# Optimization experiments

Hardware: AMD Instinct MI355X
Metric: run time of the kernel (lower is better)

## Reference

```python
import jax, jax.numpy as jnp
import numpy as np

B, N, D = 256, 8192, 768
TEMP = 0.05          # CE temperature (temp init arg; CE losses are computed but NOT returned)
SUPCON_T = 0.07      # standard SupConLoss temperature (default in the repo's SupConLoss)


def _l2norm(x, eps=1e-12):
    # matches F.normalize(dim=-1): clamp of the norm by eps
    n = jnp.linalg.norm(x, axis=-1, keepdims=True)
    return x / jnp.maximum(n, eps)


def _supcon(feats, mem, labels, mem_labels):
    # SupConLoss(features, memory, targets, prototype_labels):
    # anchor-vs-memory logits, positives where labels match prototype labels.
    logits = feats @ mem.T / SUPCON_T                              # [B, N]
    logits = logits - jax.lax.stop_gradient(logits.max(axis=1, keepdims=True))
    log_prob = logits - jax.nn.logsumexp(logits, axis=1, keepdims=True)
    mask = (labels[:, None] == mem_labels[None, :]).astype(logits.dtype)
    mean_log_prob_pos = (mask * log_prob).sum(1) / jnp.maximum(mask.sum(1), 1.0)
    return -mean_log_prob_pos.mean()


def setup_inputs() -> dict:
    key = jax.random.key(0)
    k1, k2, k3, k4, k5, k6, k7, k8 = jax.random.split(key, 8)
    inputs_rgb = jax.random.normal(k1, (B, D), dtype=jnp.float32)
    inputs_ir = jax.random.normal(k2, (B, D), dtype=jnp.float32)
    targets_rgb = jax.random.randint(k3, (B,), 0, N)
    targets_ir = jax.random.randint(k4, (B,), 0, N)
    # memory banks are unit-normalized prototypes in practice
    features_rgb = _l2norm(jax.random.normal(k5, (N, D), dtype=jnp.float32))
    features_ir = _l2norm(jax.random.normal(k6, (N, D), dtype=jnp.float32))
    # prototype labels: permutations of arange(N) so cross-modal lookups always match
    prototype_labels_rgb = jax.random.permutation(k7, jnp.arange(N))
    prototype_labels_ir = jax.random.permutation(k8, jnp.arange(N))
    return {
        "inputs_rgb": inputs_rgb, "inputs_ir": inputs_ir,
        "targets_rgb": targets_rgb, "targets_ir": targets_ir,
        "features_rgb": features_rgb, "features_ir": features_ir,
        "prototype_labels_rgb": prototype_labels_rgb,
        "prototype_labels_ir": prototype_labels_ir,
    }


def reference(inputs_rgb, inputs_ir, targets_rgb, targets_ir,
              features_rgb, features_ir, prototype_labels_rgb, prototype_labels_ir):
    x_rgb = _l2norm(inputs_rgb)
    x_ir = _l2norm(inputs_ir)
    # cm_double forward matmuls -> CE losses are computed in torch but never returned
    # (dead w.r.t. the module's outputs), so they don't affect the returned values.
    loss_contr = (_supcon(x_rgb, features_rgb, targets_rgb, prototype_labels_rgb)
                  + _supcon(x_ir, features_ir, targets_ir, prototype_labels_ir))
    loss_contr_cross = (_supcon(x_rgb, features_ir, targets_rgb, prototype_labels_ir)
                        + _supcon(x_ir, features_rgb, targets_ir, prototype_labels_rgb))
    return (loss_contr, loss_contr_cross)
```

## Files before the change

### kernel.cpp

```cpp
#include <hip/hip_runtime.h>
#include <hip/hip_bf16.h>
#include <math.h>

#define Bsz 256
#define Nsz 8192
#define Dsz 768
#define NROWS 512
#define INV_T 14.2857142857f
#define NT 64
#define NCB (Nsz / NT)
#define KC 64
#define NSTG (Dsz / KC)

typedef __attribute__((ext_vector_type(4))) float f32x4;
typedef __attribute__((ext_vector_type(8))) short bf16x8;
typedef __attribute__((ext_vector_type(4))) short bf16x4;

__device__ __forceinline__ unsigned short f2bf(float f) {
    union { float f; unsigned u; } x; x.f = f;
    unsigned u = x.u;
    return (unsigned short)((u + 0x7fffu + ((u >> 16) & 1u)) >> 16);
}
__device__ __forceinline__ float bf2f(unsigned short u) {
    union { unsigned u; float f; } x; x.u = ((unsigned)u) << 16;
    return x.f;
}

__device__ __forceinline__ int fr_idx(int row, int k) {
    int rb = row >> 4, kc = k >> 5;
    int lane = (((k >> 3) & 3) << 4) | (row & 15);
    return (((rb * 24 + kc) << 6) | lane) * 8 + (k & 7);
}

__device__ __forceinline__ bf16x8 cvt8(float4 a, float4 b) {
    union { bf16x8 v; __hip_bfloat162 h[4]; } r;
    r.h[0] = __float22bfloat162_rn({a.x, a.y});
    r.h[1] = __float22bfloat162_rn({a.z, a.w});
    r.h[2] = __float22bfloat162_rn({b.x, b.y});
    r.h[3] = __float22bfloat162_rn({b.z, b.w});
    return r.v;
}

__global__ void k_prep(const float* __restrict__ xrgb, const float* __restrict__ xir,
                       const int* __restrict__ prgb, const int* __restrict__ pir,
                       unsigned short* __restrict__ xrm, unsigned short* __restrict__ xfr,
                       int* __restrict__ inv) {
    int b = blockIdx.x, t = threadIdx.x;
    if (b < NROWS) {
        const float* src = (b < Bsz) ? (xrgb + b * Dsz) : (xir + (b - Bsz) * Dsz);
        float v0 = src[t], v1 = src[t + 256], v2 = src[t + 512];
        float ss = v0 * v0 + v1 * v1 + v2 * v2;
        #pragma unroll
        for (int m = 1; m < 64; m <<= 1) ss += __shfl_xor(ss, m);
        __shared__ float w4[4];
        if ((t & 63) == 0) w4[t >> 6] = ss;
        __syncthreads();
        float tot = w4[0] + w4[1] + w4[2] + w4[3];
        float invn = 1.0f / fmaxf(sqrtf(tot), 1e-12f);
        unsigned short b0 = f2bf(v0 * invn), b1 = f2bf(v1 * invn), b2 = f2bf(v2 * invn);
        xrm[b * Dsz + t] = b0;
        xrm[b * Dsz + t + 256] = b1;
        xrm[b * Dsz + t + 512] = b2;
        xfr[fr_idx(b, t)] = b0;
        xfr[fr_idx(b, t + 256)] = b1;
        xfr[fr_idx(b, t + 512)] = b2;
    } else {
        int i = (b - NROWS) * 256 + t;
        if (i < Nsz) inv[prgb[i]] = i;
        else         inv[Nsz + pir[i - Nsz]] = i - Nsz;
    }
}

__global__ __launch_bounds__(512) void k_big(
    const float* __restrict__ Frgb, const float* __restrict__ Fir,
    const unsigned short* __restrict__ xfr,
    float* __restrict__ part_m, float* __restrict__ part_s) {
    __shared__ short Bs[2][NT * KC];
    int bid = blockIdx.x;
    int bank = bid >> 7;
    int cb = bid & (NCB - 1);
    const float* F = bank ? Fir : Frgb;
    int t = threadIdx.x;
    int w = t >> 6, lane = t & 63, lr = lane & 15, lg = lane >> 4;

    int scol = t >> 3, sj = t & 7;
    const float* sbase = F + (long)(cb * NT + scol) * Dsz + sj * 8;
    int swidx = scol * 64 + ((sj * 8) ^ ((scol & 7) << 3));

    f32x4 acc[4][4] = {};

    {
        float4 u = *(const float4*)sbase;
        float4 v = *(const float4*)(sbase + 4);
        *(bf16x8*)&Bs[0][swidx] = cvt8(u, v);
    }
    __syncthreads();

    for (int s = 0; s < NSTG; ++s) {
        int nxt = s + 1;
        float4 un, vn;
        if (nxt < NSTG) {
            const float* p = sbase + nxt * KC;
            un = *(const float4*)p;
            vn = *(const float4*)(p + 4);
        }
        const short* B0 = Bs[s & 1];
        #pragma unroll
        for (int h = 0; h < 2; ++h) {
            int kc = s * 2 + h;
            bf16x8 bfr[4];
            #pragma unroll
            for (int cf = 0; cf < 4; ++cf) {
                int col = cf * 16 + lr;
                int kloc = h * 32 + lg * 8;
                bfr[cf] = *(const bf16x8*)&B0[col * 64 + (kloc ^ ((col & 7) << 3))];
            }
            #pragma unroll
            for (int rf = 0; rf < 4; ++rf) {
                int rb = w * 4 + rf;
                bf16x8 af = *(const bf16x8*)&xfr[(((rb * 24 + kc) << 6) | lane) * 8];
                #pragma unroll
                for (int cf = 0; cf < 4; ++cf)
                    acc[rf][cf] = __builtin_amdgcn_mfma_f32_16x16x32_bf16(af, bfr[cf], acc[rf][cf], 0, 0, 0);
            }
        }
        if (nxt < NSTG)
            *(bf16x8*)&Bs[nxt & 1][swidx] = cvt8(un, vn);
        __syncthreads();
    }

    #pragma unroll
    for (int rf = 0; rf < 4; ++rf) {
        #pragma unroll
        for (int reg = 0; reg < 4; ++reg) {
            float v0 = acc[rf][0][reg] * INV_T, v1 = acc[rf][1][reg] * INV_T;
            float v2 = acc[rf][2][reg] * INV_T, v3 = acc[rf][3][reg] * INV_T;
            float mx = fmaxf(fmaxf(v0, v1), fmaxf(v2, v3));
            mx = fmaxf(mx, __shfl_xor(mx, 1));
            mx = fmaxf(mx, __shfl_xor(mx, 2));
            mx = fmaxf(mx, __shfl_xor(mx, 4));
            mx = fmaxf(mx, __shfl_xor(mx, 8));
            float sum = __expf(v0 - mx) + __expf(v1 - mx) + __expf(v2 - mx) + __expf(v3 - mx);
            sum += __shfl_xor(sum, 1); sum += __shfl_xor(sum, 2);
            sum += __shfl_xor(sum, 4); sum += __shfl_xor(sum, 8);
            if (lr == 0) {
                int row = w * 64 + rf * 16 + lg * 4 + reg;
                long o = (long)(bank * NROWS + row) * NCB + cb;
                part_m[o] = mx;
                part_s[o] = sum;
            }
        }
    }
}

__global__ void k_combine(const float* __restrict__ part_m, const float* __restrict__ part_s,
                          const float* __restrict__ Frgb, const float* __restrict__ Fir,
                          const int* __restrict__ trgb, const int* __restrict__ tir,
                          const unsigned short* __restrict__ xrm, const int* __restrict__ inv,
                          float* __restrict__ loss) {
    int gw = (blockIdx.x * blockDim.x + threadIdx.x) >> 6;
    int lane = threadIdx.x & 63;
    int bank = gw >> 9, r = gw & 511;
    const float* pm = part_m + (long)(bank * NROWS + r) * NCB;
    const float* ps = part_s + (long)(bank * NROWS + r) * NCB;
    float m1 = pm[lane], m2 = pm[lane + 64];
    float s1 = ps[lane], s2 = ps[lane + 64];
    float m = fmaxf(m1, m2);
    float s = s1 * __expf(m1 - m) + s2 * __expf(m2 - m);
    #pragma unroll
    for (int mm = 32; mm; mm >>= 1) {
        float om = __shfl_xor(m, mm), os = __shfl_xor(s, mm);
        float nm = fmaxf(m, om);
        s = s * __expf(m - nm) + os * __expf(om - nm);
        m = nm;
    }
    int tgt = (r < Bsz) ? trgb[r] : tir[r - Bsz];
    int j = inv[bank * Nsz + tgt];
    const float* frow = (bank ? Fir : Frgb) + (long)j * Dsz;
    const unsigned short* xrow = xrm + r * Dsz;
    float d = 0.0f;
    #pragma unroll
    for (int p = 0; p < 3; ++p) {
        int k = p * 256 + lane * 4;
        bf16x4 xv = *(const bf16x4*)&xrow[k];
        float4 fv = *(const float4*)&frow[k];
        d += bf2f((unsigned short)xv[0]) * fv.x + bf2f((unsigned short)xv[1]) * fv.y
           + bf2f((unsigned short)xv[2]) * fv.z + bf2f((unsigned short)xv[3]) * fv.w;
    }
    #pragma unroll
    for (int mm = 1; mm < 64; mm <<= 1) d += __shfl_xor(d, mm);
    if (lane == 0)
        loss[gw] = (m + __logf(s)) - d * INV_T;
}

__global__ void k_final(const float* __restrict__ loss, float* __restrict__ out) {
    __shared__ float lds[1024];
    int t = threadIdx.x;
    lds[t] = loss[t];
    __syncthreads();
    for (int off = 128; off; off >>= 1) {
        if ((t & 255) < off) lds[t] += lds[t + off];
        __syncthreads();
    }
    if (t == 0) {
        out[0] = (lds[0] + lds[768]) * (1.0f / 256.0f);
        out[1] = (lds[512] + lds[256]) * (1.0f / 256.0f);
    }
}

extern "C" void kernel_launch(void* const* d_in, const int* in_sizes, int n_in,
                              void* d_out, int out_size, void* d_ws, size_t ws_size,
                              hipStream_t stream) {
    const float* in_rgb = (const float*)d_in[0];
    const float* in_ir  = (const float*)d_in[1];
    const int*   t_rgb  = (const int*)d_in[2];
    const int*   t_ir   = (const int*)d_in[3];
    const float* F_rgb  = (const float*)d_in[4];
    const float* F_ir   = (const float*)d_in[5];
    const int*   p_rgb  = (const int*)d_in[6];
    const int*   p_ir   = (const int*)d_in[7];
    float* out = (float*)d_out;
    char* ws = (char*)d_ws;

    unsigned short* xrm = (unsigned short*)ws;
    unsigned short* xfr = (unsigned short*)(ws + 786432);
    int*   inv    = (int*)  (ws + 1572864);
    float* part_m = (float*)(ws + 1638400);
    float* part_s = (float*)(ws + 2162688);
    float* loss   = (float*)(ws + 2686976);

    k_prep   <<<NROWS + 64, 256, 0, stream>>>(in_rgb, in_ir, p_rgb, p_ir, xrm, xfr, inv);
    k_big    <<<2 * NCB, 512, 0, stream>>>(F_rgb, F_ir, xfr, part_m, part_s);
    k_combine<<<256, 256, 0, stream>>>(part_m, part_s, F_rgb, F_ir, t_rgb, t_ir, xrm, inv, loss);
    k_final  <<<1, 1024, 0, stream>>>(loss, out);
}
```

Measured before the change: 126.3 us.

## Deepen global prefetch and software-pipeline A fragments; fuse final reduction via atomics

```diff
diff --git a/kernel.cpp b/kernel.cpp
--- a/kernel.cpp
+++ b/kernel.cpp
@@ -44,8 +44,9 @@
 __global__ void k_prep(const float* __restrict__ xrgb, const float* __restrict__ xir,
                        const int* __restrict__ prgb, const int* __restrict__ pir,
                        unsigned short* __restrict__ xrm, unsigned short* __restrict__ xfr,
-                       int* __restrict__ inv) {
+                       int* __restrict__ inv, float* __restrict__ out) {
     int b = blockIdx.x, t = threadIdx.x;
+    if (b == 0 && t < 2) out[t] = 0.0f;
     if (b < NROWS) {
         const float* src = (b < Bsz) ? (xrgb + b * Dsz) : (xir + (b - Bsz) * Dsz);
         float v0 = src[t], v1 = src[t + 256], v2 = src[t + 512];
@@ -89,43 +90,67 @@
 
     f32x4 acc[4][4] = {};
 
-    {
-        float4 u = *(const float4*)sbase;
-        float4 v = *(const float4*)(sbase + 4);
-        *(bf16x8*)&Bs[0][swidx] = cvt8(u, v);
-    }
+    float4 u0 = *(const float4*)sbase;
+    float4 v0 = *(const float4*)(sbase + 4);
+    float4 u1 = *(const float4*)(sbase + KC);
+    float4 v1 = *(const float4*)(sbase + KC + 4);
+    *(bf16x8*)&Bs[0][swidx] = cvt8(u0, v0);
     __syncthreads();
 
+    bf16x8 a0[4], a1[4];
+    #pragma unroll
+    for (int rf = 0; rf < 4; ++rf)
+        a0[rf] = *(const bf16x8*)&xfr[((((w * 4 + rf) * 24 + 0) << 6) | lane) * 8];
+
     for (int s = 0; s < NSTG; ++s) {
-        int nxt = s + 1;
-        float4 un, vn;
-        if (nxt < NSTG) {
-            const float* p = sbase + nxt * KC;
-            un = *(const float4*)p;
-            vn = *(const float4*)(p + 4);
+        if (s + 2 < NSTG) {
+            const float* p = sbase + (s + 2) * KC;
+            if ((s & 1) == 0) { u0 = *(const float4*)p; v0 = *(const float4*)(p + 4); }
+            else              { u1 = *(const float4*)p; v1 = *(const float4*)(p + 4); }
         }
         const short* B0 = Bs[s & 1];
-        #pragma unroll
-        for (int h = 0; h < 2; ++h) {
-            int kc = s * 2 + h;
+        {
+            int kcn = s * 2 + 1;
+            #pragma unroll
+            for (int rf = 0; rf < 4; ++rf)
+                a1[rf] = *(const bf16x8*)&xfr[((((w * 4 + rf) * 24 + kcn) << 6) | lane) * 8];
             bf16x8 bfr[4];
             #pragma unroll
             for (int cf = 0; cf < 4; ++cf) {
                 int col = cf * 16 + lr;
-                int kloc = h * 32 + lg * 8;
+                int kloc = lg * 8;
                 bfr[cf] = *(const bf16x8*)&B0[col * 64 + (kloc ^ ((col & 7) << 3))];
             }
             #pragma unroll
-            for (int rf = 0; rf < 4; ++rf) {
-                int rb = w * 4 + rf;
-                bf16x8 af = *(const bf16x8*)&xfr[(((rb * 24 + kc) << 6) | lane) * 8];
+            for (int rf = 0; rf < 4; ++rf)
                 #pragma unroll
                 for (int cf = 0; cf < 4; ++cf)
-                    acc[rf][cf] = __builtin_amdgcn_mfma_f32_16x16x32_bf16(af, bfr[cf], acc[rf][cf], 0, 0, 0);
-            }
-        }
-        if (nxt < NSTG)
-            *(bf16x8*)&Bs[nxt & 1][swidx] = cvt8(un, vn);
+                    acc[rf][cf] = __builtin_amdgcn_mfma_f32_16x16x32_bf16(a0[rf], bfr[cf], acc[rf][cf], 0, 0, 0);
+        }
+        {
+            int kcn = s * 2 + 2;
+            if (kcn < 2 * NSTG) {
+                #pragma unroll
+                for (int rf = 0; rf < 4; ++rf)
+                    a0[rf] = *(const bf16x8*)&xfr[((((w * 4 + rf) * 24 + kcn) << 6) | lane) * 8];
+            }
+            bf16x8 bfr[4];
+            #pragma unroll
+            for (int cf = 0; cf < 4; ++cf) {
+                int col = cf * 16 + lr;
+                int kloc = 32 + lg * 8;
+                bfr[cf] = *(const bf16x8*)&B0[col * 64 + (kloc ^ ((col & 7) << 3))];
+            }
+            #pragma unroll
+            for (int rf = 0; rf < 4; ++rf)
+                #pragma unroll
+                for (int cf = 0; cf < 4; ++cf)
+                    acc[rf][cf] = __builtin_amdgcn_mfma_f32_16x16x32_bf16(a1[rf], bfr[cf], acc[rf][cf], 0, 0, 0);
+        }
+        if (s + 1 < NSTG) {
+            if (((s + 1) & 1) == 0) *(bf16x8*)&Bs[0][swidx] = cvt8(u0, v0);
+            else                    *(bf16x8*)&Bs[1][swidx] = cvt8(u1, v1);
+        }
         __syncthreads();
     }
 
@@ -133,14 +158,14 @@
     for (int rf = 0; rf < 4; ++rf) {
         #pragma unroll
         for (int reg = 0; reg < 4; ++reg) {
-            float v0 = acc[rf][0][reg] * INV_T, v1 = acc[rf][1][reg] * INV_T;
-            float v2 = acc[rf][2][reg] * INV_T, v3 = acc[rf][3][reg] * INV_T;
-            float mx = fmaxf(fmaxf(v0, v1), fmaxf(v2, v3));
+            float p0 = acc[rf][0][reg] * INV_T, p1 = acc[rf][1][reg] * INV_T;
+            float p2 = acc[rf][2][reg] * INV_T, p3 = acc[rf][3][reg] * INV_T;
+            float mx = fmaxf(fmaxf(p0, p1), fmaxf(p2, p3));
             mx = fmaxf(mx, __shfl_xor(mx, 1));
             mx = fmaxf(mx, __shfl_xor(mx, 2));
             mx = fmaxf(mx, __shfl_xor(mx, 4));
             mx = fmaxf(mx, __shfl_xor(mx, 8));
-            float sum = __expf(v0 - mx) + __expf(v1 - mx) + __expf(v2 - mx) + __expf(v3 - mx);
+            float sum = __expf(p0 - mx) + __expf(p1 - mx) + __expf(p2 - mx) + __expf(p3 - mx);
             sum += __shfl_xor(sum, 1); sum += __shfl_xor(sum, 2);
             sum += __shfl_xor(sum, 4); sum += __shfl_xor(sum, 8);
             if (lr == 0) {
@@ -157,9 +182,10 @@
                           const float* __restrict__ Frgb, const float* __restrict__ Fir,
                           const int* __restrict__ trgb, const int* __restrict__ tir,
                           const unsigned short* __restrict__ xrm, const int* __restrict__ inv,
-                          float* __restrict__ loss) {
+                          float* __restrict__ out) {
     int gw = (blockIdx.x * blockDim.x + threadIdx.x) >> 6;
     int lane = threadIdx.x & 63;
+    int wl = threadIdx.x >> 6;
     int bank = gw >> 9, r = gw & 511;
     const float* pm = part_m + (long)(bank * NROWS + r) * NCB;
     const float* ps = part_s + (long)(bank * NROWS + r) * NCB;
@@ -189,22 +215,14 @@
     }
     #pragma unroll
     for (int mm = 1; mm < 64; mm <<= 1) d += __shfl_xor(d, mm);
-    if (lane == 0)
-        loss[gw] = (m + __logf(s)) - d * INV_T;
-}
-
-__global__ void k_final(const float* __restrict__ loss, float* __restrict__ out) {
-    __shared__ float lds[1024];
-    int t = threadIdx.x;
-    lds[t] = loss[t];
+
+    __shared__ float red[4];
+    if (lane == 0) red[wl] = (m + __logf(s)) - d * INV_T;
     __syncthreads();
-    for (int off = 128; off; off >>= 1) {
-        if ((t & 255) < off) lds[t] += lds[t + off];
-        __syncthreads();
-    }
-    if (t == 0) {
-        out[0] = (lds[0] + lds[768]) * (1.0f / 256.0f);
-        out[1] = (lds[512] + lds[256]) * (1.0f / 256.0f);
+    if (threadIdx.x == 0) {
+        int seg = bank ^ ((r >= Bsz) ? 1 : 0);
+        float tot = (red[0] + red[1] + red[2] + red[3]) * (1.0f / 256.0f);
+        atomicAdd(&out[seg], tot);
     }
 }
 
@@ -227,10 +245,8 @@
     int*   inv    = (int*)  (ws + 1572864);
     float* part_m = (float*)(ws + 1638400);
     float* part_s = (float*)(ws + 2162688);
-    float* loss   = (float*)(ws + 2686976);
-
-    k_prep   <<<NROWS + 64, 256, 0, stream>>>(in_rgb, in_ir, p_rgb, p_ir, xrm, xfr, inv);
+
+    k_prep   <<<NROWS + 64, 256, 0, stream>>>(in_rgb, in_ir, p_rgb, p_ir, xrm, xfr, inv, out);
     k_big    <<<2 * NCB, 512, 0, stream>>>(F_rgb, F_ir, xfr, part_m, part_s);
-    k_combine<<<256, 256, 0, stream>>>(part_m, part_s, F_rgb, F_ir, t_rgb, t_ir, xrm, inv, loss);
-    k_final  <<<1, 1024, 0, stream>>>(loss, out);
-}
+    k_combine<<<256, 256, 0, stream>>>(part_m, part_s, F_rgb, F_ir, t_rgb, t_ir, xrm, inv, out);
+}
```

After: 124.7 us. About the same (-1.3%).
